# Optimization experiments

Hardware: AMD Instinct MI355X
Metric: run time of the kernel (lower is better)

## Reference

```python
import jax, jax.numpy as jnp
import numpy as np

B, H, W = 16, 512, 512


def conv2d(x, w, b):
    # NCHW conv, stride 1, padding 1 (SAME for 3x3)
    y = jax.lax.conv_general_dilated(
        x, w, window_strides=(1, 1), padding=((1, 1), (1, 1)),
        dimension_numbers=("NCHW", "OIHW", "NCHW"))
    return y + b[None, :, None, None]


def bilinear_sample(img, py, px):
    # img: [B,H,W]; py,px: [B,K,H,W] float sample coords. Zero padding outside.
    Hh, Ww = img.shape[1], img.shape[2]
    y0 = jnp.floor(py)
    x0 = jnp.floor(px)
    wy = py - y0  # fractional weights
    wx = px - x0
    y0i = y0.astype(jnp.int32)
    x0i = x0.astype(jnp.int32)

    def gather(yi, xi):
        valid = (yi >= 0) & (yi < Hh) & (xi >= 0) & (xi < Ww)
        yc = jnp.clip(yi, 0, Hh - 1)
        xc = jnp.clip(xi, 0, Ww - 1)
        v = jax.vmap(lambda im, yy, xx: im[yy, xx])(img, yc, xc)
        return jnp.where(valid, v, jnp.zeros((), img.dtype))

    v00 = gather(y0i, x0i)
    v01 = gather(y0i, x0i + 1)
    v10 = gather(y0i + 1, x0i)
    v11 = gather(y0i + 1, x0i + 1)
    return (v00 * (1 - wy) * (1 - wx) + v01 * (1 - wy) * wx
            + v10 * wy * (1 - wx) + v11 * wy * wx)


def setup_inputs() -> dict:
    key = jax.random.key(0)
    ks = jax.random.split(key, 7)
    pm25 = jax.random.normal(ks[0], (B, 1, H, W), jnp.float32)
    avg_wind = jax.random.normal(ks[1], (B, 2, H, W), jnp.float32)
    topo = jax.random.normal(ks[2], (B, 1, H, W), jnp.float32)
    # offset_conv params (Kaiming-ish small random)
    conv1_w = jax.random.normal(ks[3], (16, 3, 3, 3), jnp.float32) * (1.0 / np.sqrt(3 * 9))
    conv1_b = jax.random.normal(ks[4], (16,), jnp.float32) * 0.01
    conv2_w = jax.random.normal(ks[5], (18, 16, 3, 3), jnp.float32) * (1.0 / np.sqrt(16 * 9))
    conv2_b = jax.random.normal(ks[6], (18,), jnp.float32) * 0.01
    # dirac init: identity 3x3 kernel
    weight = jnp.zeros((1, 1, 3, 3), jnp.float32).at[0, 0, 1, 1].set(1.0)
    return {"pm25": pm25, "avg_wind": avg_wind, "topo": topo,
            "conv1_w": conv1_w, "conv1_b": conv1_b,
            "conv2_w": conv2_w, "conv2_b": conv2_b, "weight": weight}


def reference(pm25, avg_wind, topo, conv1_w, conv1_b, conv2_w, conv2_b, weight):
    # offset-predicting conv stack
    feat = jax.nn.gelu(conv2d(jnp.concatenate([avg_wind, topo], axis=1), conv1_w, conv1_b), approximate=False)
    offsets = conv2d(feat, conv2_w, conv2_b)          # [B, 2*3*3, H, W]
    b, _, h, w = offsets.shape
    off = offsets.reshape(b, 9, 2, h, w)              # k = i*3 + j; [.,k,0]=dy, [.,k,1]=dx
    dy, dx = off[:, :, 0], off[:, :, 1]               # [B,9,H,W]

    ys = jnp.arange(h, dtype=pm25.dtype)[None, None, :, None]
    xs = jnp.arange(w, dtype=pm25.dtype)[None, None, None, :]
    ki = jnp.arange(3, dtype=pm25.dtype)
    kdy = (jnp.repeat(ki, 3) - 1.0)[None, :, None, None]  # kernel row offset - pad
    kdx = (jnp.tile(ki, 3) - 1.0)[None, :, None, None]    # kernel col offset - pad

    py = ys + kdy + dy                                # sample rows   [B,9,H,W]
    px = xs + kdx + dx                                # sample cols   [B,9,H,W]

    samp = bilinear_sample(pm25[:, 0], py, px)        # [B,9,H,W]
    wk = weight.reshape(9)                            # single-channel 3x3 kernel
    out = jnp.einsum("bkhw,k->bhw", samp, wk)[:, None]
    return out                                        # [B,1,H,W]
```

## Files before the change

kernel.cpp:

```cpp
#include <hip/hip_runtime.h>
#include <math.h>

#define Bn 16
#define Hh 512
#define Ww 512
#define HW_ (Hh * Ww)
#define TILE 32
#define NTHREADS 1024
#define FP 36
#define SIN_N 1328
#define NF 1248
#define NT1 39

typedef __bf16 bfrag __attribute__((ext_vector_type(8)));
typedef __bf16 bf4   __attribute__((ext_vector_type(4)));
typedef float  ffrag __attribute__((ext_vector_type(16)));
typedef float  f32x2 __attribute__((ext_vector_type(2)));

__device__ __forceinline__ short f2bf(float f) {
    unsigned u = __float_as_uint(f);
    unsigned r = u + 0x7FFFu + ((u >> 16) & 1u);
    return (short)(r >> 16);
}

__device__ __forceinline__ f32x2 mk2(float a, float b) { f32x2 t; t.x = a; t.y = b; return t; }

__device__ __forceinline__ f32x2 gelu_fast2(f32x2 x) {
    f32x2 z = x * x;
    f32x2 a = z * 0.044715f + 1.0f;
    f32x2 u = (x * 2.302208199f) * a;
    f32x2 e;
    e.x = __builtin_amdgcn_exp2f(u.x);
    e.y = __builtin_amdgcn_exp2f(u.y);
    f32x2 r;
    r.x = __builtin_amdgcn_rcpf(e.x + 1.0f);
    r.y = __builtin_amdgcn_rcpf(e.y + 1.0f);
    return x - x * r;
}

__device__ __forceinline__ float bilin(const float* __restrict__ img, float py, float px) {
    float y0f = floorf(py), x0f = floorf(px);
    float wy = py - y0f, wx = px - x0f;
    int y0 = (int)y0f, x0 = (int)x0f;
    auto corner = [&](int yi, int xi) -> float {
        bool valid = (yi >= 0) && (yi < Hh) && (xi >= 0) && (xi < Ww);
        int yc = min(max(yi, 0), Hh - 1);
        int xc = min(max(xi, 0), Ww - 1);
        float v = img[yc * Ww + xc];
        return valid ? v : 0.0f;
    };
    float v00 = corner(y0,     x0);
    float v01 = corner(y0,     x0 + 1);
    float v10 = corner(y0 + 1, x0);
    float v11 = corner(y0 + 1, x0 + 1);
    return (1.0f - wy) * ((1.0f - wx) * v00 + wx * v01) +
           wy          * ((1.0f - wx) * v10 + wx * v11);
}

__global__ void pack_w(const float* __restrict__ w2, const float* __restrict__ w1,
                       int* __restrict__ ws) {
    const int lane = threadIdx.x;
    const int l31  = lane & 31;
    const int lh   = lane >> 5;
    for (int tap = 0; tap < 9; ++tap) {
        int pk[4];
        #pragma unroll
        for (int jj = 0; jj < 4; ++jj) {
            float v0 = (l31 < 18) ? w2[(l31 * 16 + lh * 8 + 2 * jj    ) * 9 + tap] : 0.0f;
            float v1 = (l31 < 18) ? w2[(l31 * 16 + lh * 8 + 2 * jj + 1) * 9 + tap] : 0.0f;
            pk[jj] = ((int)(unsigned short)f2bf(v0)) | ((int)f2bf(v1) << 16);
        }
        ((int4*)ws)[tap * 64 + lane] = make_int4(pk[0], pk[1], pk[2], pk[3]);
    }
    for (int p = 0; p < 5; ++p) {
        int tap = 2 * p + lh;
        int pk[4];
        #pragma unroll
        for (int jj = 0; jj < 4; ++jj) {
            int j0 = 2 * jj, j1 = 2 * jj + 1;
            float v0 = (l31 < 16 && j0 < 3 && tap < 9) ? w1[l31 * 27 + j0 * 9 + tap] : 0.0f;
            float v1 = (l31 < 16 && j1 < 3 && tap < 9) ? w1[l31 * 27 + j1 * 9 + tap] : 0.0f;
            pk[jj] = ((int)(unsigned short)f2bf(v0)) | ((int)f2bf(v1) << 16);
        }
        ((int4*)ws)[576 + p * 64 + lane] = make_int4(pk[0], pk[1], pk[2], pk[3]);
    }
}

#define SMEM_BYTES (SIN_N * 16 + 2 * NF * 16)

__global__ __launch_bounds__(NTHREADS, 8) void residual_advection_fused(
    const float* __restrict__ pm25,
    const float* __restrict__ wind,
    const float* __restrict__ topo,
    const float* __restrict__ b1,
    const float* __restrict__ b2,
    const float* __restrict__ wt,
    const int*   __restrict__ wsB,
    float* __restrict__ out)
{
    __shared__ __align__(16) char smem[SMEM_BYTES];
    __bf16* s_in16 = (__bf16*)smem;
    __bf16* s_feat = (__bf16*)(smem + SIN_N * 16);

    const int tid = threadIdx.x;
    const int bb  = blockIdx.z;
    const int ty0 = blockIdx.y * TILE;
    const int tx0 = blockIdx.x * TILE;

    const int lane = tid & 63;
    const int wv   = tid >> 6;
    const int l31  = lane & 31;
    const int lh   = lane >> 5;

    const bfrag* WF = (const bfrag*)wsB;

    bfrag wa[5];
    #pragma unroll
    for (int p = 0; p < 5; ++p) wa[p] = WF[576 + p * 64 + lane];

    for (int idx = tid; idx < SIN_N; idx += NTHREADS) {
        float c0 = 0.0f, c1 = 0.0f, c2 = 0.0f;
        if (idx < 1296) {
            int r = idx / FP, c = idx - r * FP;
            int gy = ty0 - 2 + r, gx = tx0 - 2 + c;
            if ((unsigned)gy < (unsigned)Hh && (unsigned)gx < (unsigned)Ww) {
                int g = gy * Ww + gx;
                c0 = wind[(bb * 2 + 0) * HW_ + g];
                c1 = wind[(bb * 2 + 1) * HW_ + g];
                c2 = topo[bb * HW_ + g];
            }
        }
        bfrag v;
        v[0] = (__bf16)c0; v[1] = (__bf16)c1; v[2] = (__bf16)c2; v[3] = (__bf16)0.0f;
        v[4] = (__bf16)0.0f; v[5] = (__bf16)0.0f; v[6] = (__bf16)0.0f; v[7] = (__bf16)0.0f;
        *(bfrag*)&s_in16[idx * 8] = v;
    }
    __syncthreads();

    {
        int off1[5];
        #pragma unroll
        for (int p = 0; p < 5; ++p) {
            int t0 = 2 * p, t1 = (2 * p + 1 < 9) ? 2 * p + 1 : 0;
            int o0 = (t0 / 3) * FP + t0 % 3;
            int o1 = (t1 / 3) * FP + t1 % 3;
            off1[p] = lh ? o1 : o0;
        }
        const float4 ba  = *(const float4*)&b1[4 * lh];
        const float4 bb4 = *(const float4*)&b1[8 + 4 * lh];

        for (int tt = wv; tt < NT1; tt += 16) {
            const int m0 = tt * 32 + l31;
            ffrag acc;
            #pragma unroll
            for (int r = 0; r < 16; ++r) acc[r] = 0.0f;
            #pragma unroll
            for (int p = 0; p < 5; ++p) {
                bfrag bx = *(const bfrag*)&s_in16[(m0 + off1[p]) * 8];
                acc = __builtin_amdgcn_mfma_f32_32x32x16_bf16(wa[p], bx, acc, 0, 0, 0);
            }
            int fyp = m0 / FP;
            int fxp = m0 - fyp * FP;
            int gy = ty0 + fyp - 1, gx = tx0 + fxp - 1;
            float msk = ((unsigned)gy < (unsigned)Hh && (unsigned)gx < (unsigned)Ww) ? 1.0f : 0.0f;
            f32x2 g0 = gelu_fast2(mk2(acc[0] + ba.x,  acc[1] + ba.y))  * msk;
            f32x2 g1 = gelu_fast2(mk2(acc[2] + ba.z,  acc[3] + ba.w))  * msk;
            f32x2 g2 = gelu_fast2(mk2(acc[4] + bb4.x, acc[5] + bb4.y)) * msk;
            f32x2 g3 = gelu_fast2(mk2(acc[6] + bb4.z, acc[7] + bb4.w)) * msk;
            bf4 wlo, whi;
            wlo[0] = (__bf16)g0.x; wlo[1] = (__bf16)g0.y; wlo[2] = (__bf16)g1.x; wlo[3] = (__bf16)g1.y;
            whi[0] = (__bf16)g2.x; whi[1] = (__bf16)g2.y; whi[2] = (__bf16)g3.x; whi[3] = (__bf16)g3.y;
            *(bf4*)&s_feat[m0 * 8 + lh * 4]        = wlo;
            *(bf4*)&s_feat[(NF + m0) * 8 + lh * 4] = whi;
        }
    }
    __syncthreads();

    ffrag a0, a1;
    #pragma unroll
    for (int r = 0; r < 16; ++r) { a0[r] = 0.0f; a1[r] = 0.0f; }
    {
        const int base0 = (2 * wv) * FP + l31;
        #pragma unroll
        for (int t = 0; t < 9; ++t) {
            const int toff = (t / 3) * FP + (t % 3);
            bfrag wf = WF[t * 64 + lane];
            bfrag f0 = *(const bfrag*)&s_feat[(lh * NF + base0 + toff) * 8];
            bfrag f1 = *(const bfrag*)&s_feat[(lh * NF + base0 + FP + toff) * 8];
            a0 = __builtin_amdgcn_mfma_f32_32x32x16_bf16(wf, f0, a0, 0, 0, 0);
            a1 = __builtin_amdgcn_mfma_f32_32x32x16_bf16(wf, f1, a1, 0, 0, 0);
        }
    }

    {
        const float* img = pm25 + bb * HW_;
        const float fy0 = (float)(ty0 + 2 * wv);
        const float fx  = (float)(tx0 + l31);
        float o0 = 0.0f, o1 = 0.0f;
        constexpr int T0[5] = {0, 1, 4, 5, 8};
        constexpr int T1[5] = {2, 3, 6, 7, 0};
        #pragma unroll
        for (int i = 0; i < 5; ++i) {
            const int t0 = T0[i], t1 = T1[i];
            float wk  = lh ? ((i < 4) ? wt[t1] : 0.0f) : wt[t0];
            float bdy = lh ? b2[2 * t1]     : b2[2 * t0];
            float bdx = lh ? b2[2 * t1 + 1] : b2[2 * t0 + 1];
            float kdy = lh ? (float)(t1 / 3 - 1) : (float)(t0 / 3 - 1);
            float kdx = lh ? (float)(t1 % 3 - 1) : (float)(t0 % 3 - 1);
            if (wk != 0.0f) {
                float dy0 = a0[2 * i] + bdy, dx0 = a0[2 * i + 1] + bdx;
                float dy1 = a1[2 * i] + bdy, dx1 = a1[2 * i + 1] + bdx;
                o0 += wk * bilin(img, fy0 + kdy + dy0,        fx + kdx + dx0);
                o1 += wk * bilin(img, fy0 + 1.0f + kdy + dy1, fx + kdx + dx1);
            }
        }
        o0 += __shfl_xor(o0, 32);
        o1 += __shfl_xor(o1, 32);
        float ov = lh ? o1 : o0;
        out[bb * HW_ + (ty0 + 2 * wv + lh) * Ww + (tx0 + l31)] = ov;
    }
}

extern "C" void kernel_launch(void* const* d_in, const int* in_sizes, int n_in,
                              void* d_out, int out_size, void* d_ws, size_t ws_size,
                              hipStream_t stream) {
    const float* pm25 = (const float*)d_in[0];
    const float* wind = (const float*)d_in[1];
    const float* topo = (const float*)d_in[2];
    const float* w1   = (const float*)d_in[3];
    const float* b1   = (const float*)d_in[4];
    const float* w2   = (const float*)d_in[5];
    const float* b2   = (const float*)d_in[6];
    const float* wt   = (const float*)d_in[7];
    float* o          = (float*)d_out;
    int*   wsB        = (int*)d_ws;

    pack_w<<<dim3(1), dim3(64), 0, stream>>>(w2, w1, wsB);

    dim3 grid(Ww / TILE, Hh / TILE, Bn);
    residual_advection_fused<<<grid, dim3(NTHREADS), 0, stream>>>(
        pm25, wind, topo, b1, b2, wt, wsB, o);
}
```

Measured before the change: 196.6 us.

## Recast first conv as 16x16x32 MFMA with folded bias and redistribute bilinear taps

The first convolution now uses 16x16x32 bf16 MFMA. Each K slice packs a 2x4 spatial window of 4 channels, the fourth channel being a constant one that carries the folded conv1 bias. This cuts it from five 32x32 MFMAs per tile to two smaller ones. The input staging uses a 37-wide padded layout with overlapping half-vector stores, and the GELU mask is applied only on edge tiles. The sampling stage now exchanges offset rows across half-waves with shuffles, so each lane samples all nine taps for its own pixel, and the bilinear corner code is simplified. The risks are extra shuffle and select overhead, and the first-layer bias now being rounded to bf16.

```diff
diff --git a/kernel.cpp b/kernel.cpp
--- a/kernel.cpp
+++ b/kernel.cpp
@@ -7,14 +7,15 @@
 #define HW_ (Hh * Ww)
 #define TILE 32
 #define NTHREADS 1024
-#define FP 36
-#define SIN_N 1328
-#define NF 1248
-#define NT1 39
+#define S 37
+#define SIN_N 1400
+#define NFP 1280
+#define NT2 80
 
 typedef __bf16 bfrag __attribute__((ext_vector_type(8)));
 typedef __bf16 bf4   __attribute__((ext_vector_type(4)));
 typedef float  ffrag __attribute__((ext_vector_type(16)));
+typedef float  f32x4 __attribute__((ext_vector_type(4)));
 typedef float  f32x2 __attribute__((ext_vector_type(2)));
 
 __device__ __forceinline__ short f2bf(float f) {
@@ -42,23 +43,22 @@
     float y0f = floorf(py), x0f = floorf(px);
     float wy = py - y0f, wx = px - x0f;
     int y0 = (int)y0f, x0 = (int)x0f;
-    auto corner = [&](int yi, int xi) -> float {
-        bool valid = (yi >= 0) && (yi < Hh) && (xi >= 0) && (xi < Ww);
-        int yc = min(max(yi, 0), Hh - 1);
-        int xc = min(max(xi, 0), Ww - 1);
-        float v = img[yc * Ww + xc];
-        return valid ? v : 0.0f;
-    };
-    float v00 = corner(y0,     x0);
-    float v01 = corner(y0,     x0 + 1);
-    float v10 = corner(y0 + 1, x0);
-    float v11 = corner(y0 + 1, x0 + 1);
+    int yc0 = min(max(y0, 0), Hh - 1), yc1 = min(max(y0 + 1, 0), Hh - 1);
+    int xc0 = min(max(x0, 0), Ww - 1), xc1 = min(max(x0 + 1, 0), Ww - 1);
+    bool vy0 = (unsigned)y0 < (unsigned)Hh, vy1 = (unsigned)(y0 + 1) < (unsigned)Hh;
+    bool vx0 = (unsigned)x0 < (unsigned)Ww, vx1 = (unsigned)(x0 + 1) < (unsigned)Ww;
+    const float* r0 = img + yc0 * Ww;
+    const float* r1 = img + yc1 * Ww;
+    float v00 = (vy0 && vx0) ? r0[xc0] : 0.0f;
+    float v01 = (vy0 && vx1) ? r0[xc1] : 0.0f;
+    float v10 = (vy1 && vx0) ? r1[xc0] : 0.0f;
+    float v11 = (vy1 && vx1) ? r1[xc1] : 0.0f;
     return (1.0f - wy) * ((1.0f - wx) * v00 + wx * v01) +
            wy          * ((1.0f - wx) * v10 + wx * v11);
 }
 
 __global__ void pack_w(const float* __restrict__ w2, const float* __restrict__ w1,
-                       int* __restrict__ ws) {
+                       const float* __restrict__ b1, int* __restrict__ ws) {
     const int lane = threadIdx.x;
     const int l31  = lane & 31;
     const int lh   = lane >> 5;
@@ -72,40 +72,49 @@
         }
         ((int4*)ws)[tap * 64 + lane] = make_int4(pk[0], pk[1], pk[2], pk[3]);
     }
-    for (int p = 0; p < 5; ++p) {
-        int tap = 2 * p + lh;
+    const int m  = lane & 15;
+    const int kq = lane >> 4;
+    for (int t = 0; t < 2; ++t) {
         int pk[4];
         #pragma unroll
         for (int jj = 0; jj < 4; ++jj) {
-            int j0 = 2 * jj, j1 = 2 * jj + 1;
-            float v0 = (l31 < 16 && j0 < 3 && tap < 9) ? w1[l31 * 27 + j0 * 9 + tap] : 0.0f;
-            float v1 = (l31 < 16 && j1 < 3 && tap < 9) ? w1[l31 * 27 + j1 * 9 + tap] : 0.0f;
-            pk[jj] = ((int)(unsigned short)f2bf(v0)) | ((int)f2bf(v1) << 16);
-        }
-        ((int4*)ws)[576 + p * 64 + lane] = make_int4(pk[0], pk[1], pk[2], pk[3]);
-    }
-}
-
-#define SMEM_BYTES (SIN_N * 16 + 2 * NF * 16)
+            float vv[2];
+            #pragma unroll
+            for (int h = 0; h < 2; ++h) {
+                int k   = kq * 8 + 2 * jj + h;
+                int kyl = k >> 4, kx = (k >> 2) & 3, c = k & 3;
+                int ky  = 2 * t + kyl;
+                float x = 0.0f;
+                if (kx < 3 && c < 3 && ky < 3) x = w1[m * 27 + c * 9 + ky * 3 + kx];
+                if (t == 0 && k == 3) x = b1[m];
+                vv[h] = x;
+            }
+            pk[jj] = ((int)(unsigned short)f2bf(vv[0])) | ((int)f2bf(vv[1]) << 16);
+        }
+        ((int4*)ws)[576 + t * 64 + lane] = make_int4(pk[0], pk[1], pk[2], pk[3]);
+    }
+}
+
+#define SMEM_BYTES (SIN_N * 16 + 2 * NFP * 16)
 
 __global__ __launch_bounds__(NTHREADS, 8) void residual_advection_fused(
     const float* __restrict__ pm25,
     const float* __restrict__ wind,
     const float* __restrict__ topo,
-    const float* __restrict__ b1,
     const float* __restrict__ b2,
     const float* __restrict__ wt,
     const int*   __restrict__ wsB,
     float* __restrict__ out)
 {
     __shared__ __align__(16) char smem[SMEM_BYTES];
-    __bf16* s_in16 = (__bf16*)smem;
+    __bf16* s_in   = (__bf16*)smem;
     __bf16* s_feat = (__bf16*)(smem + SIN_N * 16);
 
     const int tid = threadIdx.x;
     const int bb  = blockIdx.z;
     const int ty0 = blockIdx.y * TILE;
     const int tx0 = blockIdx.x * TILE;
+    const bool edge = (ty0 == 0) || (ty0 == Hh - TILE) || (tx0 == 0) || (tx0 == Ww - TILE);
 
     const int lane = tid & 63;
     const int wv   = tid >> 6;
@@ -114,14 +123,13 @@
 
     const bfrag* WF = (const bfrag*)wsB;
 
-    bfrag wa[5];
-    #pragma unroll
-    for (int p = 0; p < 5; ++p) wa[p] = WF[576 + p * 64 + lane];
+    bfrag w1f0 = WF[576 + lane];
+    bfrag w1f1 = WF[640 + lane];
 
     for (int idx = tid; idx < SIN_N; idx += NTHREADS) {
         float c0 = 0.0f, c1 = 0.0f, c2 = 0.0f;
-        if (idx < 1296) {
-            int r = idx / FP, c = idx - r * FP;
+        if (idx < 36 * S) {
+            int r = idx / S, c = idx - r * S;
             int gy = ty0 - 2 + r, gx = tx0 - 2 + c;
             if ((unsigned)gy < (unsigned)Hh && (unsigned)gx < (unsigned)Ww) {
                 int g = gy * Ww + gx;
@@ -130,48 +138,40 @@
                 c2 = topo[bb * HW_ + g];
             }
         }
-        bfrag v;
-        v[0] = (__bf16)c0; v[1] = (__bf16)c1; v[2] = (__bf16)c2; v[3] = (__bf16)0.0f;
-        v[4] = (__bf16)0.0f; v[5] = (__bf16)0.0f; v[6] = (__bf16)0.0f; v[7] = (__bf16)0.0f;
-        *(bfrag*)&s_in16[idx * 8] = v;
+        bf4 v;
+        v[0] = (__bf16)c0; v[1] = (__bf16)c1; v[2] = (__bf16)c2; v[3] = (__bf16)1.0f;
+        *(bf4*)&s_in[idx * 8] = v;
+        if (idx > 0) *(bf4*)&s_in[idx * 8 - 4] = v;
     }
     __syncthreads();
 
     {
-        int off1[5];
-        #pragma unroll
-        for (int p = 0; p < 5; ++p) {
-            int t0 = 2 * p, t1 = (2 * p + 1 < 9) ? 2 * p + 1 : 0;
-            int o0 = (t0 / 3) * FP + t0 % 3;
-            int o1 = (t1 / 3) * FP + t1 % 3;
-            off1[p] = lh ? o1 : o0;
-        }
-        const float4 ba  = *(const float4*)&b1[4 * lh];
-        const float4 bb4 = *(const float4*)&b1[8 + 4 * lh];
-
-        for (int tt = wv; tt < NT1; tt += 16) {
-            const int m0 = tt * 32 + l31;
-            ffrag acc;
-            #pragma unroll
-            for (int r = 0; r < 16; ++r) acc[r] = 0.0f;
-            #pragma unroll
-            for (int p = 0; p < 5; ++p) {
-                bfrag bx = *(const bfrag*)&s_in16[(m0 + off1[p]) * 8];
-                acc = __builtin_amdgcn_mfma_f32_32x32x16_bf16(wa[p], bx, acc, 0, 0, 0);
-            }
-            int fyp = m0 / FP;
-            int fxp = m0 - fyp * FP;
-            int gy = ty0 + fyp - 1, gx = tx0 + fxp - 1;
-            float msk = ((unsigned)gy < (unsigned)Hh && (unsigned)gx < (unsigned)Ww) ? 1.0f : 0.0f;
-            f32x2 g0 = gelu_fast2(mk2(acc[0] + ba.x,  acc[1] + ba.y))  * msk;
-            f32x2 g1 = gelu_fast2(mk2(acc[2] + ba.z,  acc[3] + ba.w))  * msk;
-            f32x2 g2 = gelu_fast2(mk2(acc[4] + bb4.x, acc[5] + bb4.y)) * msk;
-            f32x2 g3 = gelu_fast2(mk2(acc[6] + bb4.z, acc[7] + bb4.w)) * msk;
-            bf4 wlo, whi;
-            wlo[0] = (__bf16)g0.x; wlo[1] = (__bf16)g0.y; wlo[2] = (__bf16)g1.x; wlo[3] = (__bf16)g1.y;
-            whi[0] = (__bf16)g2.x; whi[1] = (__bf16)g2.y; whi[2] = (__bf16)g3.x; whi[3] = (__bf16)g3.y;
-            *(bf4*)&s_feat[m0 * 8 + lh * 4]        = wlo;
-            *(bf4*)&s_feat[(NF + m0) * 8 + lh * 4] = whi;
+        const int n    = lane & 15;
+        const int kq   = lane >> 4;
+        const int qoff = (kq >> 1) * S + (kq & 1) * 2;
+        #pragma unroll
+        for (int i = 0; i < 5; ++i) {
+            const int p = (wv * 5 + i) * 16 + n;
+            f32x4 acc;
+            acc[0] = 0.0f; acc[1] = 0.0f; acc[2] = 0.0f; acc[3] = 0.0f;
+            bfrag bx0 = *(const bfrag*)&s_in[(p + qoff) * 8];
+            bfrag bx1 = *(const bfrag*)&s_in[(p + qoff + 2 * S) * 8];
+            acc = __builtin_amdgcn_mfma_f32_16x16x32_bf16(w1f0, bx0, acc, 0, 0, 0);
+            acc = __builtin_amdgcn_mfma_f32_16x16x32_bf16(w1f1, bx1, acc, 0, 0, 0);
+            f32x2 g0 = gelu_fast2(mk2(acc[0], acc[1]));
+            f32x2 g1 = gelu_fast2(mk2(acc[2], acc[3]));
+            if (edge) {
+                int fy = p / S;
+                int fx = p - fy * S;
+                int gy = ty0 + fy - 1, gx = tx0 + fx - 1;
+                float msk = ((unsigned)gy < (unsigned)Hh && (unsigned)gx < (unsigned)Ww)
+                            ? 1.0f : 0.0f;
+                g0 *= msk; g1 *= msk;
+            }
+            bf4 w4;
+            w4[0] = (__bf16)g0.x; w4[1] = (__bf16)g0.y;
+            w4[2] = (__bf16)g1.x; w4[3] = (__bf16)g1.y;
+            *(bf4*)&s_feat[((kq >> 1) * NFP + p) * 8 + (kq & 1) * 4] = w4;
         }
     }
     __syncthreads();
@@ -180,44 +180,51 @@
     #pragma unroll
     for (int r = 0; r < 16; ++r) { a0[r] = 0.0f; a1[r] = 0.0f; }
     {
-        const int base0 = (2 * wv) * FP + l31;
+        const int vb = (lh * NFP + (2 * wv) * S + l31) * 8;
         #pragma unroll
         for (int t = 0; t < 9; ++t) {
-            const int toff = (t / 3) * FP + (t % 3);
+            const int toff = ((t / 3) * S + (t % 3)) * 8;
             bfrag wf = WF[t * 64 + lane];
-            bfrag f0 = *(const bfrag*)&s_feat[(lh * NF + base0 + toff) * 8];
-            bfrag f1 = *(const bfrag*)&s_feat[(lh * NF + base0 + FP + toff) * 8];
+            bfrag f0 = *(const bfrag*)&s_feat[vb + toff];
+            bfrag f1 = *(const bfrag*)&s_feat[vb + toff + S * 8];
             a0 = __builtin_amdgcn_mfma_f32_32x32x16_bf16(wf, f0, a0, 0, 0, 0);
             a1 = __builtin_amdgcn_mfma_f32_32x32x16_bf16(wf, f1, a1, 0, 0, 0);
         }
     }
 
     {
+        float ex[10];
+        #pragma unroll
+        for (int j = 0; j < 10; ++j) {
+            float snd = lh ? a0[(j < 8) ? j : 7] : a1[j];
+            ex[j] = __shfl_xor(snd, 32);
+        }
+        auto getv = [&](int row) -> float {
+            if ((row & 4) == 0) {
+                int r = (row < 8) ? row : ((row < 16) ? row - 4 : row - 8);
+                return lh ? ex[r] : a0[r];
+            } else {
+                int r = (row & 3) + 4 * (row >> 3);
+                return lh ? a1[r] : ex[r];
+            }
+        };
         const float* img = pm25 + bb * HW_;
-        const float fy0 = (float)(ty0 + 2 * wv);
-        const float fx  = (float)(tx0 + l31);
-        float o0 = 0.0f, o1 = 0.0f;
-        constexpr int T0[5] = {0, 1, 4, 5, 8};
-        constexpr int T1[5] = {2, 3, 6, 7, 0};
-        #pragma unroll
-        for (int i = 0; i < 5; ++i) {
-            const int t0 = T0[i], t1 = T1[i];
-            float wk  = lh ? ((i < 4) ? wt[t1] : 0.0f) : wt[t0];
-            float bdy = lh ? b2[2 * t1]     : b2[2 * t0];
-            float bdx = lh ? b2[2 * t1 + 1] : b2[2 * t0 + 1];
-            float kdy = lh ? (float)(t1 / 3 - 1) : (float)(t0 / 3 - 1);
-            float kdx = lh ? (float)(t1 % 3 - 1) : (float)(t0 % 3 - 1);
+        const int py_i = ty0 + 2 * wv + lh;
+        const int px_i = tx0 + l31;
+        const float fy = (float)py_i, fx = (float)px_i;
+        float o = 0.0f;
+        #pragma unroll
+        for (int t = 0; t < 9; ++t) {
+            float wk = wt[t];
             if (wk != 0.0f) {
-                float dy0 = a0[2 * i] + bdy, dx0 = a0[2 * i + 1] + bdx;
-                float dy1 = a1[2 * i] + bdy, dx1 = a1[2 * i + 1] + bdx;
-                o0 += wk * bilin(img, fy0 + kdy + dy0,        fx + kdx + dx0);
-                o1 += wk * bilin(img, fy0 + 1.0f + kdy + dy1, fx + kdx + dx1);
-            }
-        }
-        o0 += __shfl_xor(o0, 32);
-        o1 += __shfl_xor(o1, 32);
-        float ov = lh ? o1 : o0;
-        out[bb * HW_ + (ty0 + 2 * wv + lh) * Ww + (tx0 + l31)] = ov;
+                float dy = getv(2 * t)     + b2[2 * t];
+                float dx = getv(2 * t + 1) + b2[2 * t + 1];
+                float py = fy + (float)(t / 3 - 1) + dy;
+                float px = fx + (float)(t % 3 - 1) + dx;
+                o += wk * bilin(img, py, px);
+            }
+        }
+        out[bb * HW_ + py_i * Ww + px_i] = o;
     }
 }
 
@@ -235,9 +242,9 @@
     float* o          = (float*)d_out;
     int*   wsB        = (int*)d_ws;
 
-    pack_w<<<dim3(1), dim3(64), 0, stream>>>(w2, w1, wsB);
+    pack_w<<<dim3(1), dim3(64), 0, stream>>>(w2, w1, b1, wsB);
 
     dim3 grid(Ww / TILE, Hh / TILE, Bn);
     residual_advection_fused<<<grid, dim3(NTHREADS), 0, stream>>>(
-        pm25, wind, topo, b1, b2, wt, wsB, o);
-}
+        pm25, wind, topo, b2, wt, wsB, o);
+}
```

Result: faster. 176.8 us (-10.0%).
